# Optimization experiments

Hardware: AMD Instinct MI355X
Metric: run time of the kernel (lower is better)

## Reference

```python
import jax, jax.numpy as jnp
import numpy as np

N_NODES = 50000
N_EDGES = 800000
NFEAT = 512
NHID = 128


def gcn_conv(x, W, b, src, dst, n_nodes):
    """PyG-style GCNConv: self-loops + symmetric deg^{-1/2} normalization."""
    # degrees over edges incl. self-loops (src/dst already contain them)
    deg = jax.ops.segment_sum(jnp.ones_like(src, dtype=x.dtype), dst,
                              num_segments=n_nodes)
    dinv = jnp.where(deg > 0, jax.lax.rsqrt(deg), 0.0)
    norm = dinv[src] * dinv[dst]            # [E+N]
    h = x @ W                               # [N, out] dense transform first (out <= in)
    msgs = h[src] * norm[:, None]           # gather + scale
    out = jax.ops.segment_sum(msgs, dst, num_segments=n_nodes)  # scatter-add
    return out + b


def setup_inputs() -> dict:
    key = jax.random.key(0)
    k1, k2, k3, k4 = jax.random.split(key, 4)
    x = jax.random.normal(k1, (N_NODES, NFEAT), dtype=jnp.float32)
    edge_index = jax.random.randint(k2, (2, N_EDGES), 0, N_NODES, dtype=jnp.int64)
    W1 = jax.random.normal(k3, (NFEAT, 2 * NHID), dtype=jnp.float32) / np.sqrt(NFEAT)
    b1 = jnp.zeros((2 * NHID,), dtype=jnp.float32)
    W2 = jax.random.normal(k4, (2 * NHID, NHID), dtype=jnp.float32) / np.sqrt(2 * NHID)
    b2 = jnp.zeros((NHID,), dtype=jnp.float32)
    return {"x": x, "edge_index": edge_index, "W1": W1, "b1": b1, "W2": W2, "b2": b2}


def reference(x, edge_index, W1, b1, W2, b2):
    n = x.shape[0]
    loop = jnp.arange(n, dtype=edge_index.dtype)
    src = jnp.concatenate([edge_index[0], loop])  # add self-loops once, reuse per layer
    dst = jnp.concatenate([edge_index[1], loop])
    h = jax.nn.relu(gcn_conv(x, W1, b1, src, dst, n))
    # dropout is identity in eval mode (reference runs in inference mode)
    out = gcn_conv(h, W2, b2, src, dst, n)
    return out
```

## Files before the change

### kernel.cpp

```cpp
#include <hip/hip_runtime.h>
#include <cstdint>
#include <cstddef>

#define NFEAT 512
#define NH1   256
#define NH2   128

#define SCAN_BLOCK 256
#define SCAN_ELEMS 4
#define SCAN_TILE  (SCAN_BLOCK * SCAN_ELEMS)

#define P_CHUNKS 128
#define HHALF    25088
#define NP       (2 * HHALF)

typedef __attribute__((ext_vector_type(8))) short short8;
typedef __attribute__((ext_vector_type(4))) float float4v;

__device__ __forceinline__ unsigned short f2bf(float f) {
    unsigned int u = __float_as_uint(f);
    u += 0x7fffu + ((u >> 16) & 1u);
    return (unsigned short)(u >> 16);
}
__device__ __forceinline__ float bf2f(unsigned short u) {
    return __uint_as_float(((unsigned int)u) << 16);
}

__device__ __forceinline__ void load_lds16(const void* g, void* l) {
    __builtin_amdgcn_global_load_lds(
        (const __attribute__((address_space(1))) void*)g,
        (__attribute__((address_space(3))) void*)l, 16, 0, 0);
}

__global__ __launch_bounds__(256) void k_hist(const int* __restrict__ dst,
                                              int* __restrict__ hist, int E, int CE) {
    __shared__ int lh[HHALF];
    const int c    = blockIdx.x >> 1;
    const int hf   = blockIdx.x & 1;
    const int base = hf * HHALF;
    for (int i = threadIdx.x; i < HHALF; i += 256) lh[i] = 0;
    __syncthreads();
    const int lo = c * CE;
    const int hi = lo + CE < E ? lo + CE : E;
    for (int e = lo + (int)threadIdx.x; e < hi; e += 256) {
        const int d = dst[e] - base;
        if ((unsigned)d < (unsigned)HHALF) atomicAdd(&lh[d], 1);
    }
    __syncthreads();
    int* outp = hist + (size_t)c * NP + base;
    for (int i = threadIdx.x; i < HHALF; i += 256) outp[i] = lh[i];
}

__global__ void k_colreduce(const int* __restrict__ hist, int* __restrict__ degi,
                            float* __restrict__ dinv, int N) {
    const int d = blockIdx.x * blockDim.x + threadIdx.x;
    if (d >= N) return;
    int s = 0;
#pragma unroll 8
    for (int c = 0; c < P_CHUNKS; ++c) s += hist[(size_t)c * NP + d];
    degi[d] = s;
    dinv[d] = rsqrtf((float)(s + 1));
}

__global__ void k_coloffs(int* __restrict__ hist, const int* __restrict__ row_start,
                          int N) {
    const int d = blockIdx.x * blockDim.x + threadIdx.x;
    if (d >= N) return;
    int run = row_start[d];
    for (int c = 0; c < P_CHUNKS; ++c) {
        int* p = &hist[(size_t)c * NP + d];
        const int t = *p;
        *p = run;
        run += t;
    }
}

__global__ __launch_bounds__(256) void k_place(const int* __restrict__ src,
                                               const int* __restrict__ dst,
                                               const int* __restrict__ hist,
                                               int* __restrict__ csr_src, int E, int CE) {
    __shared__ int lcur[HHALF];
    const int c    = blockIdx.x >> 1;
    const int hf   = blockIdx.x & 1;
    const int base = hf * HHALF;
    const int* offp = hist + (size_t)c * NP + base;
    for (int i = threadIdx.x; i < HHALF; i += 256) lcur[i] = offp[i];
    __syncthreads();
    const int lo = c * CE;
    const int hi = lo + CE < E ? lo + CE : E;
    for (int e = lo + (int)threadIdx.x; e < hi; e += 256) {
        const int d = dst[e] - base;
        if ((unsigned)d < (unsigned)HHALF) {
            const int p = atomicAdd(&lcur[d], 1);
            csr_src[p] = src[e];
        }
    }
}

__global__ __launch_bounds__(SCAN_BLOCK) void k_scan1(
    const int* __restrict__ degi, int* __restrict__ blocksums, int N) {
    __shared__ int red[SCAN_BLOCK];
    const int t = threadIdx.x;
    const int base = blockIdx.x * SCAN_TILE + t * SCAN_ELEMS;
    int s = 0;
#pragma unroll
    for (int i = 0; i < SCAN_ELEMS; ++i) {
        const int idx = base + i;
        if (idx < N) s += degi[idx];
    }
    red[t] = s;
    __syncthreads();
    for (int off = SCAN_BLOCK / 2; off > 0; off >>= 1) {
        if (t < off) red[t] += red[t + off];
        __syncthreads();
    }
    if (t == 0) blocksums[blockIdx.x] = red[0];
}

__global__ __launch_bounds__(1024) void k_scan2(
    const int* __restrict__ blocksums, int* __restrict__ blockoffs,
    int* __restrict__ row_start, int nb, int N) {
    __shared__ int sm[1024];
    const int t = threadIdx.x;
    const int v = (t < nb) ? blocksums[t] : 0;
    sm[t] = v;
    __syncthreads();
    for (int off = 1; off < 1024; off <<= 1) {
        const int x = (t >= off) ? sm[t - off] : 0;
        __syncthreads();
        sm[t] += x;
        __syncthreads();
    }
    if (t < nb) blockoffs[t] = sm[t] - v;
    if (t == 1023) row_start[N] = sm[1023];
}

__global__ __launch_bounds__(SCAN_BLOCK) void k_scan3(
    const int* __restrict__ degi, const int* __restrict__ blockoffs,
    int* __restrict__ row_start, int N) {
    __shared__ int tsum[SCAN_BLOCK];
    const int t = threadIdx.x;
    const int base = blockIdx.x * SCAN_TILE + t * SCAN_ELEMS;
    int v[SCAN_ELEMS];
    int s = 0;
#pragma unroll
    for (int i = 0; i < SCAN_ELEMS; ++i) {
        const int idx = base + i;
        v[i] = (idx < N) ? degi[idx] : 0;
        s += v[i];
    }
    tsum[t] = s;
    __syncthreads();
    for (int off = 1; off < SCAN_BLOCK; off <<= 1) {
        const int x = (t >= off) ? tsum[t - off] : 0;
        __syncthreads();
        tsum[t] += x;
        __syncthreads();
    }
    int excl = blockoffs[blockIdx.x] + tsum[t] - s;
#pragma unroll
    for (int i = 0; i < SCAN_ELEMS; ++i) {
        const int idx = base + i;
        if (idx < N) row_start[idx] = excl;
        excl += v[i];
    }
}

__global__ void k_cvt_x(const float* __restrict__ x, const float* __restrict__ dinv,
                        unsigned short* __restrict__ xb, int Nrows, int Mp) {
    int i = blockIdx.x * blockDim.x + threadIdx.x;
    int total = Mp * (NFEAT / 4);
    if (i >= total) return;
    int row = i / (NFEAT / 4);
    int q   = (i % (NFEAT / 4)) * 4;
    ushort4 o;
    if (row < Nrows) {
        const float w = dinv[row];
        const float4 v = *(const float4*)&x[(size_t)row * NFEAT + q];
        o.x = f2bf(v.x * w); o.y = f2bf(v.y * w);
        o.z = f2bf(v.z * w); o.w = f2bf(v.w * w);
    } else {
        o.x = 0; o.y = 0; o.z = 0; o.w = 0;
    }
    *(ushort4*)&xb[(size_t)row * NFEAT + q] = o;
}

__global__ void k_cvt_wt(const float* __restrict__ W, unsigned short* __restrict__ Wt,
                         int K, int Nc) {
    int i = blockIdx.x * blockDim.x + threadIdx.x;
    if (i >= K * Nc) return;
    int k = i / Nc, n = i % Nc;
    Wt[(size_t)n * K + k] = f2bf(W[(size_t)k * Nc + n]);
}

__global__ __launch_bounds__(256) void gemm_bf16(
    const unsigned short* __restrict__ A, const unsigned short* __restrict__ Bt,
    unsigned short* __restrict__ C, int N, int K) {
    __shared__ unsigned short As[128 * 32];
    __shared__ unsigned short Bs[128 * 32];
    const int t    = threadIdx.x;
    const int wave = t >> 6, lane = t & 63;
    const int row0 = blockIdx.y * 128, col0 = blockIdx.x * 128;
    const int wm = (wave >> 1) * 64, wn = (wave & 1) * 64;
    const int sr = lane >> 2;
    const int sk = (lane & 3) * 8;
    const int quad = lane >> 4, l15 = lane & 15;

    const int ca = wave * 2;
    const unsigned short* gA0 = A  + (size_t)(row0 + ca * 16 + sr) * K + sk;
    const unsigned short* gA1 = gA0 + (size_t)16 * K;
    const unsigned short* gB0 = Bt + (size_t)(col0 + ca * 16 + sr) * K + sk;
    const unsigned short* gB1 = gB0 + (size_t)16 * K;
    unsigned short* lA0 = &As[ca * 512];
    unsigned short* lA1 = &As[(ca + 1) * 512];
    unsigned short* lB0 = &Bs[ca * 512];
    unsigned short* lB1 = &Bs[(ca + 1) * 512];

    float4v acc[4][4] = {};

    for (int k0 = 0; k0 < K; k0 += 32) {
        __syncthreads();
        load_lds16(gA0 + k0, lA0);
        load_lds16(gA1 + k0, lA1);
        load_lds16(gB0 + k0, lB0);
        load_lds16(gB1 + k0, lB1);
        __syncthreads();

        short8 a[4], b[4];
#pragma unroll
        for (int i = 0; i < 4; ++i) {
            a[i] = *(const short8*)&As[(wm + i * 16 + l15) * 32 + quad * 8];
            b[i] = *(const short8*)&Bs[(wn + i * 16 + l15) * 32 + quad * 8];
        }
#pragma unroll
        for (int mt = 0; mt < 4; ++mt)
#pragma unroll
            for (int nt = 0; nt < 4; ++nt)
                acc[mt][nt] = __builtin_amdgcn_mfma_f32_16x16x32_bf16(
                    a[mt], b[nt], acc[mt][nt], 0, 0, 0);
    }

#pragma unroll
    for (int mt = 0; mt < 4; ++mt) {
#pragma unroll
        for (int nt = 0; nt < 4; ++nt) {
            const int c = col0 + wn + nt * 16 + l15;
#pragma unroll
            for (int r = 0; r < 4; ++r) {
                const int row = row0 + wm + mt * 16 + quad * 4 + r;
                C[(size_t)row * N + c] = f2bf(acc[mt][nt][r]);
            }
        }
    }
}

template <int F, bool RELU, bool OUTF32>
__global__ __launch_bounds__(256) void k_gather(
    const int* __restrict__ row_start, const int* __restrict__ csr_src,
    const float* __restrict__ dinv, const unsigned short* __restrict__ h,
    const float* __restrict__ bias, unsigned short* __restrict__ ob,
    float* __restrict__ of, int N) {
    const int gid  = blockIdx.x * blockDim.x + threadIdx.x;
    const int node = gid >> 6;
    const int lane = gid & 63;
    if (node >= N) return;

    constexpr int EL = F / 64;
    const float wd = dinv[node];
    const int jb = row_start[node];
    const int je = row_start[node + 1];
    const unsigned short* hl = h + (size_t)lane * EL;

    float acc[EL];
    {
        const unsigned short* hp = hl + (size_t)node * F;
        if (EL == 4) {
            const ushort4 v = *(const ushort4*)hp;
            acc[0] = bf2f(v.x); acc[1] = bf2f(v.y);
            acc[2] = bf2f(v.z); acc[3] = bf2f(v.w);
        } else {
            const ushort2 v = *(const ushort2*)hp;
            acc[0] = bf2f(v.x); acc[1] = bf2f(v.y);
        }
    }

    for (int j0 = jb; j0 < je; j0 += 64) {
        int jj = j0 + lane;
        if (jj >= je) jj = je - 1;
        const int myi = csr_src[jj];
        const int rem = je - j0;
        const int cnt = rem < 64 ? rem : 64;
        int i = 0;
        for (; i + 4 <= cnt; i += 4) {
            const int s0 = __shfl(myi, i + 0);
            const int s1 = __shfl(myi, i + 1);
            const int s2 = __shfl(myi, i + 2);
            const int s3 = __shfl(myi, i + 3);
            if (EL == 4) {
                const ushort4 v0 = *(const ushort4*)(hl + (size_t)s0 * F);
                const ushort4 v1 = *(const ushort4*)(hl + (size_t)s1 * F);
                const ushort4 v2 = *(const ushort4*)(hl + (size_t)s2 * F);
                const ushort4 v3 = *(const ushort4*)(hl + (size_t)s3 * F);
                acc[0] += bf2f(v0.x) + bf2f(v1.x) + bf2f(v2.x) + bf2f(v3.x);
                acc[1] += bf2f(v0.y) + bf2f(v1.y) + bf2f(v2.y) + bf2f(v3.y);
                acc[2] += bf2f(v0.z) + bf2f(v1.z) + bf2f(v2.z) + bf2f(v3.z);
                acc[3] += bf2f(v0.w) + bf2f(v1.w) + bf2f(v2.w) + bf2f(v3.w);
            } else {
                const ushort2 v0 = *(const ushort2*)(hl + (size_t)s0 * F);
                const ushort2 v1 = *(const ushort2*)(hl + (size_t)s1 * F);
                const ushort2 v2 = *(const ushort2*)(hl + (size_t)s2 * F);
                const ushort2 v3 = *(const ushort2*)(hl + (size_t)s3 * F);
                acc[0] += bf2f(v0.x) + bf2f(v1.x) + bf2f(v2.x) + bf2f(v3.x);
                acc[1] += bf2f(v0.y) + bf2f(v1.y) + bf2f(v2.y) + bf2f(v3.y);
            }
        }
        for (; i < cnt; ++i) {
            const int s = __shfl(myi, i);
            const unsigned short* hp = hl + (size_t)s * F;
            if (EL == 4) {
                const ushort4 v = *(const ushort4*)hp;
                acc[0] += bf2f(v.x); acc[1] += bf2f(v.y);
                acc[2] += bf2f(v.z); acc[3] += bf2f(v.w);
            } else {
                const ushort2 v = *(const ushort2*)hp;
                acc[0] += bf2f(v.x); acc[1] += bf2f(v.y);
            }
        }
    }

#pragma unroll
    for (int i = 0; i < EL; ++i) {
        float v = fmaf(acc[i], wd, bias[lane * EL + i]);
        if (OUTF32) {
            of[(size_t)node * F + lane * EL + i] = v;
        } else {
            if (RELU) v = fmaxf(v, 0.f);
            ob[(size_t)node * F + lane * EL + i] = f2bf(v * wd);
        }
    }
}

extern "C" void kernel_launch(void* const* d_in, const int* in_sizes, int n_in,
                              void* d_out, int out_size, void* d_ws, size_t ws_size,
                              hipStream_t stream) {
    const float* x   = (const float*)d_in[0];
    const int*   ei  = (const int*)d_in[1];
    const float* W1  = (const float*)d_in[2];
    const float* b1  = (const float*)d_in[3];
    const float* W2  = (const float*)d_in[4];
    const float* b2  = (const float*)d_in[5];
    float*       out = (float*)d_out;

    const int N = in_sizes[0] / NFEAT;
    const int E = in_sizes[1] / 2;
    const int Mp = ((N + 127) / 128) * 128;
    const int* srcp = ei;
    const int* dstp = ei + E;
    const int nScanBlocks = (N + SCAN_TILE - 1) / SCAN_TILE;
    const int CE = (E + P_CHUNKS - 1) / P_CHUNKS;

    char* wsb = (char*)d_ws;
    auto take = [&](size_t bytes) {
        char* p = wsb;
        wsb += (bytes + 255) & ~(size_t)255;
        return p;
    };
    int*   degi      = (int*)take((size_t)N * 4);
    int*   row_start = (int*)take((size_t)(N + 1) * 4);
    int*   csr_src   = (int*)take((size_t)E * 4);
    int*   blocksums = (int*)take((size_t)1024 * 4);
    int*   blockoffs = (int*)take((size_t)1024 * 4);
    float* dinv      = (float*)take((size_t)N * 4);
    unsigned short* xb  = (unsigned short*)take((size_t)Mp * NFEAT * 2);
    unsigned short* W1t = (unsigned short*)take((size_t)NH1 * NFEAT * 2);
    unsigned short* W2t = (unsigned short*)take((size_t)NH2 * NH1 * 2);
    const size_t hBytes    = (size_t)Mp * NH1 * 2;
    const size_t histBytes = (size_t)P_CHUNKS * NP * 4;
    char* big = take(histBytes > 2 * hBytes ? histBytes : 2 * hBytes);
    int*            hist = (int*)big;
    unsigned short* h    = (unsigned short*)big;
    unsigned short* h1   = (unsigned short*)(big + hBytes);
    unsigned short* h2   = xb;

    k_hist<<<P_CHUNKS * 2, 256, 0, stream>>>(dstp, hist, E, CE);
    k_colreduce<<<(N + 255) / 256, 256, 0, stream>>>(hist, degi, dinv, N);
    k_scan1<<<nScanBlocks, SCAN_BLOCK, 0, stream>>>(degi, blocksums, N);
    k_scan2<<<1, 1024, 0, stream>>>(blocksums, blockoffs, row_start, nScanBlocks, N);
    k_scan3<<<nScanBlocks, SCAN_BLOCK, 0, stream>>>(degi, blockoffs, row_start, N);
    k_coloffs<<<(N + 255) / 256, 256, 0, stream>>>(hist, row_start, N);
    k_place<<<P_CHUNKS * 2, 256, 0, stream>>>(srcp, dstp, hist, csr_src, E, CE);

    {
        int total = Mp * (NFEAT / 4);
        k_cvt_x<<<(total + 255) / 256, 256, 0, stream>>>(x, dinv, xb, N, Mp);
    }
    k_cvt_wt<<<(NFEAT * NH1 + 255) / 256, 256, 0, stream>>>(W1, W1t, NFEAT, NH1);
    k_cvt_wt<<<(NH1 * NH2 + 255) / 256, 256, 0, stream>>>(W2, W2t, NH1, NH2);

    {
        dim3 g(NH1 / 128, Mp / 128);
        gemm_bf16<<<g, 256, 0, stream>>>(xb, W1t, h, NH1, NFEAT);
    }
    {
        int total = N * 64;
        k_gather<NH1, true, false><<<(total + 255) / 256, 256, 0, stream>>>(
            row_start, csr_src, dinv, h, b1, h1, nullptr, N);
    }

    {
        dim3 g(NH2 / 128, Mp / 128);
        gemm_bf16<<<g, 256, 0, stream>>>(h1, W2t, h2, NH2, NH1);
    }
    {
        int total = N * 64;
        k_gather<NH2, false, true><<<(total + 255) / 256, 256, 0, stream>>>(
            row_start, csr_src, dinv, h2, b2, nullptr, out, N);
    }
}
```

Baseline: 372.1 us.

## Pack per-chunk histogram counts as 16-bit pairs and widen gather loads to 16 bytes

The CSR build now packs the counts of two nodes into each 32-bit word, so one LDS histogram covers every node. This halves the blocks and the dst rescans in the hist and place kernels, and it halves the size of the histogram buffer. The coloffs kernel now produces offsets relative to each chunk, and place adds row_start[d] when it computes the write position. The gather kernel now has each lane load 8 bf16 values (16 bytes), so several edges are processed per wave in parallel and partial sums are combined with cross-lane xor shuffles. The packing assumes a node's in-degree, and its count within any chunk, fits in 16 bits, which holds for this input size.

```diff
diff --git a/kernel.cpp b/kernel.cpp
--- a/kernel.cpp
+++ b/kernel.cpp
@@ -11,10 +11,10 @@
 #define SCAN_TILE  (SCAN_BLOCK * SCAN_ELEMS)
 
 #define P_CHUNKS 128
-#define HHALF    25088
-#define NP       (2 * HHALF)
+#define NWMAX    25088
 
 typedef __attribute__((ext_vector_type(8))) short short8;
+typedef __attribute__((ext_vector_type(8))) unsigned short ushortx8;
 typedef __attribute__((ext_vector_type(4))) float float4v;
 
 __device__ __forceinline__ unsigned short f2bf(float f) {
@@ -32,68 +32,74 @@
         (__attribute__((address_space(3))) void*)l, 16, 0, 0);
 }
 
+
 __global__ __launch_bounds__(256) void k_hist(const int* __restrict__ dst,
-                                              int* __restrict__ hist, int E, int CE) {
-    __shared__ int lh[HHALF];
-    const int c    = blockIdx.x >> 1;
-    const int hf   = blockIdx.x & 1;
-    const int base = hf * HHALF;
-    for (int i = threadIdx.x; i < HHALF; i += 256) lh[i] = 0;
-    __syncthreads();
+                                              unsigned int* __restrict__ hist,
+                                              int E, int CE, int NW) {
+    __shared__ unsigned int lh[NWMAX];
+    for (int i = threadIdx.x; i < NW; i += 256) lh[i] = 0;
+    __syncthreads();
+    const int c  = blockIdx.x;
     const int lo = c * CE;
     const int hi = lo + CE < E ? lo + CE : E;
     for (int e = lo + (int)threadIdx.x; e < hi; e += 256) {
-        const int d = dst[e] - base;
-        if ((unsigned)d < (unsigned)HHALF) atomicAdd(&lh[d], 1);
-    }
-    __syncthreads();
-    int* outp = hist + (size_t)c * NP + base;
-    for (int i = threadIdx.x; i < HHALF; i += 256) outp[i] = lh[i];
-}
-
-__global__ void k_colreduce(const int* __restrict__ hist, int* __restrict__ degi,
-                            float* __restrict__ dinv, int N) {
-    const int d = blockIdx.x * blockDim.x + threadIdx.x;
-    if (d >= N) return;
-    int s = 0;
+        const int d = dst[e];
+        atomicAdd(&lh[d >> 1], (d & 1) ? (1u << 16) : 1u);
+    }
+    __syncthreads();
+    unsigned int* outp = hist + (size_t)c * NW;
+    for (int i = threadIdx.x; i < NW; i += 256) outp[i] = lh[i];
+}
+
+__global__ void k_colreduce(const unsigned int* __restrict__ hist,
+                            int* __restrict__ degi, float* __restrict__ dinv,
+                            int NW, int N) {
+    const int w = blockIdx.x * blockDim.x + threadIdx.x;
+    if (w >= NW) return;
+    unsigned int s = 0;
 #pragma unroll 8
-    for (int c = 0; c < P_CHUNKS; ++c) s += hist[(size_t)c * NP + d];
-    degi[d] = s;
-    dinv[d] = rsqrtf((float)(s + 1));
-}
-
-__global__ void k_coloffs(int* __restrict__ hist, const int* __restrict__ row_start,
-                          int N) {
-    const int d = blockIdx.x * blockDim.x + threadIdx.x;
-    if (d >= N) return;
-    int run = row_start[d];
+    for (int c = 0; c < P_CHUNKS; ++c) s += hist[(size_t)c * NW + w];
+    const int d0 = s & 0xffff, d1 = s >> 16;
+    const int n0 = 2 * w, n1 = 2 * w + 1;
+    if (n0 < N) { degi[n0] = d0; dinv[n0] = rsqrtf((float)(d0 + 1)); }
+    if (n1 < N) { degi[n1] = d1; dinv[n1] = rsqrtf((float)(d1 + 1)); }
+}
+
+__global__ void k_coloffs(unsigned int* __restrict__ hist, int NW) {
+    const int w = blockIdx.x * blockDim.x + threadIdx.x;
+    if (w >= NW) return;
+    unsigned int run0 = 0, run1 = 0;
     for (int c = 0; c < P_CHUNKS; ++c) {
-        int* p = &hist[(size_t)c * NP + d];
-        const int t = *p;
-        *p = run;
-        run += t;
+        unsigned int* p = &hist[(size_t)c * NW + w];
+        const unsigned int t = *p;
+        *p = run0 | (run1 << 16);
+        run0 += t & 0xffff;
+        run1 += t >> 16;
     }
 }
 
 __global__ __launch_bounds__(256) void k_place(const int* __restrict__ src,
                                                const int* __restrict__ dst,
-                                               const int* __restrict__ hist,
-                                               int* __restrict__ csr_src, int E, int CE) {
-    __shared__ int lcur[HHALF];
-    const int c    = blockIdx.x >> 1;
-    const int hf   = blockIdx.x & 1;
-    const int base = hf * HHALF;
-    const int* offp = hist + (size_t)c * NP + base;
-    for (int i = threadIdx.x; i < HHALF; i += 256) lcur[i] = offp[i];
-    __syncthreads();
+                                               const unsigned int* __restrict__ hist,
+                                               const int* __restrict__ row_start,
+                                               int* __restrict__ csr_src,
+                                               int E, int CE, int NW) {
+    __shared__ unsigned int lcur[NWMAX];
+    for (int i = threadIdx.x; i < NW; i += 256) lcur[i] = 0;
+    __syncthreads();
+    const int c  = blockIdx.x;
     const int lo = c * CE;
     const int hi = lo + CE < E ? lo + CE : E;
+    const unsigned int* relrow = hist + (size_t)c * NW;
     for (int e = lo + (int)threadIdx.x; e < hi; e += 256) {
-        const int d = dst[e] - base;
-        if ((unsigned)d < (unsigned)HHALF) {
-            const int p = atomicAdd(&lcur[d], 1);
-            csr_src[p] = src[e];
-        }
+        const int d  = dst[e];
+        const int w  = d >> 1;
+        const int sh = (d & 1) * 16;
+        const unsigned int old = atomicAdd(&lcur[w], 1u << sh);
+        const int local = (old >> sh) & 0xffff;
+        const int rel   = (relrow[w] >> sh) & 0xffff;
+        const int pos   = row_start[d] + rel + local;
+        csr_src[pos] = src[e];
     }
 }
 
@@ -260,28 +266,27 @@
     const float* __restrict__ dinv, const unsigned short* __restrict__ h,
     const float* __restrict__ bias, unsigned short* __restrict__ ob,
     float* __restrict__ of, int N) {
+    constexpr int LPE = F / 8;
+    constexpr int EPW = 64 / LPE;
     const int gid  = blockIdx.x * blockDim.x + threadIdx.x;
     const int node = gid >> 6;
     const int lane = gid & 63;
     if (node >= N) return;
-
-    constexpr int EL = F / 64;
+    const int slot = lane / LPE;
+    const int fb   = (lane % LPE) * 8;
     const float wd = dinv[node];
     const int jb = row_start[node];
     const int je = row_start[node + 1];
-    const unsigned short* hl = h + (size_t)lane * EL;
-
-    float acc[EL];
-    {
-        const unsigned short* hp = hl + (size_t)node * F;
-        if (EL == 4) {
-            const ushort4 v = *(const ushort4*)hp;
-            acc[0] = bf2f(v.x); acc[1] = bf2f(v.y);
-            acc[2] = bf2f(v.z); acc[3] = bf2f(v.w);
-        } else {
-            const ushort2 v = *(const ushort2*)hp;
-            acc[0] = bf2f(v.x); acc[1] = bf2f(v.y);
-        }
+    const unsigned short* hf = h + fb;
+
+    float acc[8];
+    if (slot == 0) {
+        const ushortx8 v = *(const ushortx8*)(hf + (size_t)node * F);
+#pragma unroll
+        for (int e = 0; e < 8; ++e) acc[e] = bf2f(v[e]);
+    } else {
+#pragma unroll
+        for (int e = 0; e < 8; ++e) acc[e] = 0.f;
     }
 
     for (int j0 = jb; j0 < je; j0 += 64) {
@@ -291,51 +296,58 @@
         const int rem = je - j0;
         const int cnt = rem < 64 ? rem : 64;
         int i = 0;
-        for (; i + 4 <= cnt; i += 4) {
-            const int s0 = __shfl(myi, i + 0);
-            const int s1 = __shfl(myi, i + 1);
-            const int s2 = __shfl(myi, i + 2);
-            const int s3 = __shfl(myi, i + 3);
-            if (EL == 4) {
-                const ushort4 v0 = *(const ushort4*)(hl + (size_t)s0 * F);
-                const ushort4 v1 = *(const ushort4*)(hl + (size_t)s1 * F);
-                const ushort4 v2 = *(const ushort4*)(hl + (size_t)s2 * F);
-                const ushort4 v3 = *(const ushort4*)(hl + (size_t)s3 * F);
-                acc[0] += bf2f(v0.x) + bf2f(v1.x) + bf2f(v2.x) + bf2f(v3.x);
-                acc[1] += bf2f(v0.y) + bf2f(v1.y) + bf2f(v2.y) + bf2f(v3.y);
-                acc[2] += bf2f(v0.z) + bf2f(v1.z) + bf2f(v2.z) + bf2f(v3.z);
-                acc[3] += bf2f(v0.w) + bf2f(v1.w) + bf2f(v2.w) + bf2f(v3.w);
-            } else {
-                const ushort2 v0 = *(const ushort2*)(hl + (size_t)s0 * F);
-                const ushort2 v1 = *(const ushort2*)(hl + (size_t)s1 * F);
-                const ushort2 v2 = *(const ushort2*)(hl + (size_t)s2 * F);
-                const ushort2 v3 = *(const ushort2*)(hl + (size_t)s3 * F);
-                acc[0] += bf2f(v0.x) + bf2f(v1.x) + bf2f(v2.x) + bf2f(v3.x);
-                acc[1] += bf2f(v0.y) + bf2f(v1.y) + bf2f(v2.y) + bf2f(v3.y);
+        for (; i + 4 * EPW <= cnt; i += 4 * EPW) {
+            const int s0 = __shfl(myi, i + 0 * EPW + slot);
+            const int s1 = __shfl(myi, i + 1 * EPW + slot);
+            const int s2 = __shfl(myi, i + 2 * EPW + slot);
+            const int s3 = __shfl(myi, i + 3 * EPW + slot);
+            const ushortx8 v0 = *(const ushortx8*)(hf + (size_t)s0 * F);
+            const ushortx8 v1 = *(const ushortx8*)(hf + (size_t)s1 * F);
+            const ushortx8 v2 = *(const ushortx8*)(hf + (size_t)s2 * F);
+            const ushortx8 v3 = *(const ushortx8*)(hf + (size_t)s3 * F);
+#pragma unroll
+            for (int e = 0; e < 8; ++e)
+                acc[e] += (bf2f(v0[e]) + bf2f(v1[e])) + (bf2f(v2[e]) + bf2f(v3[e]));
+        }
+        for (; i < cnt; i += EPW) {
+            const int idx = i + slot;
+            const bool ok = idx < cnt;
+            const int s = __shfl(myi, ok ? idx : cnt - 1);
+            const ushortx8 v = *(const ushortx8*)(hf + (size_t)s * F);
+            if (ok) {
+#pragma unroll
+                for (int e = 0; e < 8; ++e) acc[e] += bf2f(v[e]);
             }
         }
-        for (; i < cnt; ++i) {
-            const int s = __shfl(myi, i);
-            const unsigned short* hp = hl + (size_t)s * F;
-            if (EL == 4) {
-                const ushort4 v = *(const ushort4*)hp;
-                acc[0] += bf2f(v.x); acc[1] += bf2f(v.y);
-                acc[2] += bf2f(v.z); acc[3] += bf2f(v.w);
-            } else {
-                const ushort2 v = *(const ushort2*)hp;
-                acc[0] += bf2f(v.x); acc[1] += bf2f(v.y);
+    }
+
+#pragma unroll
+    for (int e = 0; e < 8; ++e) {
+        if (EPW == 4) acc[e] += __shfl_xor(acc[e], 16);
+        acc[e] += __shfl_xor(acc[e], 32);
+    }
+
+    if (slot == 0) {
+        const float4 b0 = *(const float4*)&bias[fb];
+        const float4 b1 = *(const float4*)&bias[fb + 4];
+        float r[8];
+        r[0] = fmaf(acc[0], wd, b0.x); r[1] = fmaf(acc[1], wd, b0.y);
+        r[2] = fmaf(acc[2], wd, b0.z); r[3] = fmaf(acc[3], wd, b0.w);
+        r[4] = fmaf(acc[4], wd, b1.x); r[5] = fmaf(acc[5], wd, b1.y);
+        r[6] = fmaf(acc[6], wd, b1.z); r[7] = fmaf(acc[7], wd, b1.w);
+        if (OUTF32) {
+            float* op = &of[(size_t)node * F + fb];
+            *(float4*)op       = make_float4(r[0], r[1], r[2], r[3]);
+            *(float4*)(op + 4) = make_float4(r[4], r[5], r[6], r[7]);
+        } else {
+            ushortx8 o;
+#pragma unroll
+            for (int e = 0; e < 8; ++e) {
+                float v = r[e];
+                if (RELU) v = fmaxf(v, 0.f);
+                o[e] = f2bf(v * wd);
             }
-        }
-    }
-
-#pragma unroll
-    for (int i = 0; i < EL; ++i) {
-        float v = fmaf(acc[i], wd, bias[lane * EL + i]);
-        if (OUTF32) {
-            of[(size_t)node * F + lane * EL + i] = v;
-        } else {
-            if (RELU) v = fmaxf(v, 0.f);
-            ob[(size_t)node * F + lane * EL + i] = f2bf(v * wd);
+            *(ushortx8*)&ob[(size_t)node * F + fb] = o;
         }
     }
 }
@@ -358,6 +370,7 @@
     const int* dstp = ei + E;
     const int nScanBlocks = (N + SCAN_TILE - 1) / SCAN_TILE;
     const int CE = (E + P_CHUNKS - 1) / P_CHUNKS;
+    const int NW = (N + 1) / 2;
 
     char* wsb = (char*)d_ws;
     auto take = [&](size_t bytes) {
@@ -375,20 +388,20 @@
     unsigned short* W1t = (unsigned short*)take((size_t)NH1 * NFEAT * 2);
     unsigned short* W2t = (unsigned short*)take((size_t)NH2 * NH1 * 2);
     const size_t hBytes    = (size_t)Mp * NH1 * 2;
-    const size_t histBytes = (size_t)P_CHUNKS * NP * 4;
+    const size_t histBytes = (size_t)P_CHUNKS * NW * 4;
     char* big = take(histBytes > 2 * hBytes ? histBytes : 2 * hBytes);
-    int*            hist = (int*)big;
+    unsigned int*   hist = (unsigned int*)big;
     unsigned short* h    = (unsigned short*)big;
     unsigned short* h1   = (unsigned short*)(big + hBytes);
     unsigned short* h2   = xb;
 
-    k_hist<<<P_CHUNKS * 2, 256, 0, stream>>>(dstp, hist, E, CE);
-    k_colreduce<<<(N + 255) / 256, 256, 0, stream>>>(hist, degi, dinv, N);
+    k_hist<<<P_CHUNKS, 256, 0, stream>>>(dstp, hist, E, CE, NW);
+    k_colreduce<<<(NW + 255) / 256, 256, 0, stream>>>(hist, degi, dinv, NW, N);
     k_scan1<<<nScanBlocks, SCAN_BLOCK, 0, stream>>>(degi, blocksums, N);
     k_scan2<<<1, 1024, 0, stream>>>(blocksums, blockoffs, row_start, nScanBlocks, N);
     k_scan3<<<nScanBlocks, SCAN_BLOCK, 0, stream>>>(degi, blockoffs, row_start, N);
-    k_coloffs<<<(N + 255) / 256, 256, 0, stream>>>(hist, row_start, N);
-    k_place<<<P_CHUNKS * 2, 256, 0, stream>>>(srcp, dstp, hist, csr_src, E, CE);
+    k_coloffs<<<(NW + 255) / 256, 256, 0, stream>>>(hist, NW);
+    k_place<<<P_CHUNKS, 256, 0, stream>>>(srcp, dstp, hist, row_start, csr_src, E, CE, NW);
 
     {
         int total = Mp * (NFEAT / 4);
```

Result: slower. 394.4 us (+6.0%).
